# Kernel optimization log

Measured on AMD Instinct MI355X. Metric: run time of the kernel, lower is better.

The kernel has to match this reference:

```python
import jax, jax.numpy as jnp
import numpy as np


def setup_inputs() -> dict:
    key = jax.random.key(0)
    k_x, k_w, k_b = jax.random.split(key, 3)
    B, F, D, H = 4096, 64, 128, 4
    inputs = jax.random.normal(k_x, (B, F, D), dtype=jnp.float32)
    w = jax.random.normal(k_w, (H, D), dtype=jnp.float32)
    b = jax.random.normal(k_b, (H,), dtype=jnp.float32)
    return {"inputs": inputs, "w": w, "b": b}


def reference(inputs, w, b):
    # pairwise outer-product contracted with head weights:
    # scores[b,i,j,h] = sum_d x[b,i,d] * x[b,j,d] * w[h,d]
    scores = jnp.einsum('bid,bjd,hd->bijh', inputs, inputs, w) + b  # [B,F,F,H]
    s = jnp.sum(scores, axis=-1)  # [B,F,F]
    denom = jnp.sum(s, axis=(1, 2), keepdims=True)  # [B,1,1]
    return s / denom
```

## Files before the change

kernel.cpp:

```cpp
#include <hip/hip_runtime.h>
#include <hip/hip_bf16.h>


constexpr int F = 64;
constexpr int D = 128;

using bf16x8 = __attribute__((ext_vector_type(8))) short;
using f32x4  = __attribute__((ext_vector_type(4))) float;

__device__ __forceinline__ int tile_addr(int chunk, int row) {
    return ((((chunk << 6) + row) << 4) ^ ((chunk & 7) << 4));
}

__device__ __forceinline__ unsigned pk2(float lo, float hi) {
    float2 f2; f2.x = lo; f2.y = hi;
    __hip_bfloat162 h = __float22bfloat162_rn(f2);
    union { __hip_bfloat162 h2; unsigned u; } cv; cv.h2 = h;
    return cv.u;
}
__device__ __forceinline__ float lo16f(unsigned u) { return __uint_as_float(u << 16); }
__device__ __forceinline__ float hi16f(unsigned u) { return __uint_as_float(u & 0xFFFF0000u); }

__global__ __launch_bounds__(256, 8) void afm_kernel(
    const float* __restrict__ x, const float* __restrict__ w,
    const float* __restrict__ bias, float* __restrict__ out)
{
    __shared__ short sB[F * D];
    __shared__ float sW[D];
    __shared__ float sSp[4][D];

    const int t    = threadIdx.x;
    const int blk  = blockIdx.x;
    const int lane = t & 63;
    const int wv   = t >> 6;

    if (t < D) sW[t] = w[t] + w[D + t] + w[2 * D + t] + w[3 * D + t];
    const float bsum = bias[0] + bias[1] + bias[2] + bias[3];

    const float* xb = x + (size_t)blk * (F * D);
    const int col   = (4 * t) & 127;
    const int chunk = col >> 3;
    const int ebyte = (col & 7) << 1;
    float c0 = 0.f, c1 = 0.f, c2 = 0.f, c3 = 0.f;
    char* sBc = reinterpret_cast<char*>(sB);

    #pragma unroll
    for (int k = 0; k < 8; ++k) {
        const int f   = k * 1024 + 4 * t;
        const int row = f >> 7;
        const float4 v = *reinterpret_cast<const float4*>(xb + f);
        c0 += v.x; c1 += v.y; c2 += v.z; c3 += v.w;
        uint2 pb; pb.x = pk2(v.x, v.y); pb.y = pk2(v.z, v.w);
        *reinterpret_cast<uint2*>(sBc + tile_addr(chunk, row) + ebyte) = pb;
    }
    c0 += __shfl_xor(c0, 32, 64); c1 += __shfl_xor(c1, 32, 64);
    c2 += __shfl_xor(c2, 32, 64); c3 += __shfl_xor(c3, 32, 64);
    if (lane < 32) {
        float4 cs; cs.x = c0; cs.y = c1; cs.z = c2; cs.w = c3;
        *reinterpret_cast<float4*>(&sSp[wv][col]) = cs;
    }
    __syncthreads();

    const float S0 = sSp[0][lane] + sSp[1][lane] + sSp[2][lane] + sSp[3][lane];
    const float S1 = sSp[0][64 + lane] + sSp[1][64 + lane] + sSp[2][64 + lane] + sSp[3][64 + lane];
    float p = S0 * S0 * sW[lane] + S1 * S1 * sW[64 + lane];
    #pragma unroll
    for (int off = 32; off; off >>= 1) p += __shfl_xor(p, off, 64);

    f32x4 acc[4] = {{0,0,0,0},{0,0,0,0},{0,0,0,0},{0,0,0,0}};
    const int fr   = lane & 15;
    const int kgrp = lane >> 4;
    const int r_a  = wv * 16 + fr;

    #pragma unroll
    for (int s = 0; s < 4; ++s) {
        const int ch = 4 * s + kgrp;
        const uint4  raw = *reinterpret_cast<const uint4*>(sBc + tile_addr(ch, r_a));
        const float4 wa  = *reinterpret_cast<const float4*>(&sW[ch * 8]);
        const float4 wb  = *reinterpret_cast<const float4*>(&sW[ch * 8 + 4]);
        union { uint4 u; bf16x8 v; } af;
        af.u.x = pk2(lo16f(raw.x) * wa.x, hi16f(raw.x) * wa.y);
        af.u.y = pk2(lo16f(raw.y) * wa.z, hi16f(raw.y) * wa.w);
        af.u.z = pk2(lo16f(raw.z) * wb.x, hi16f(raw.z) * wb.y);
        af.u.w = pk2(lo16f(raw.w) * wb.z, hi16f(raw.w) * wb.w);
        #pragma unroll
        for (int tj = 0; tj < 4; ++tj) {
            union { uint4 u; bf16x8 v; } bf;
            bf.u = *reinterpret_cast<const uint4*>(sBc + tile_addr(ch, tj * 16 + fr));
            acc[tj] = __builtin_amdgcn_mfma_f32_16x16x32_bf16(af.v, bf.v, acc[tj], 0, 0, 0);
        }
    }

    const float rden  = 1.0f / (p + 4096.0f * bsum);
    const int   rbase = wv * 16 + 4 * kgrp;
    float* ob = out + (size_t)blk * (F * F);
    #pragma unroll
    for (int tj = 0; tj < 4; ++tj) {
        float4 o;
        o.x = (acc[tj][0] + bsum) * rden;
        o.y = (acc[tj][1] + bsum) * rden;
        o.z = (acc[tj][2] + bsum) * rden;
        o.w = (acc[tj][3] + bsum) * rden;
        *reinterpret_cast<float4*>(ob + (size_t)(tj * 16 + fr) * F + rbase) = o;
    }
}

extern "C" void kernel_launch(void* const* d_in, const int* in_sizes, int n_in,
                              void* d_out, int out_size, void* d_ws, size_t ws_size,
                              hipStream_t stream) {
    const float* x  = (const float*)d_in[0];
    const float* w  = (const float*)d_in[1];
    const float* b  = (const float*)d_in[2];
    float* out      = (float*)d_out;

    afm_kernel<<<4096, 256, 0, stream>>>(x, w, b, out);
}
```

Before: 36.02 us.

## Stage fp32 inputs into LDS via direct global-to-LDS loads with swizzle

Replaces the register path (global load, bf16 pack, LDS store) with asynchronous global_load_lds of raw fp32 rows into a swizzled LDS tile. Column sums and the bf16 conversion now read from LDS, and the B operand is converted to bf16 inside the MFMA loop. LDS use doubles to 32KB per block, so the occupancy hint is lowered to 4 blocks. The intent is to cut VGPR staging and instruction overhead on the load path, at the cost of extra LDS reads, repeated conversions of B fragments, and lower occupancy.

```diff
diff --git a/kernel.cpp b/kernel.cpp
--- a/kernel.cpp
+++ b/kernel.cpp
@@ -8,91 +8,98 @@
 using bf16x8 = __attribute__((ext_vector_type(8))) short;
 using f32x4  = __attribute__((ext_vector_type(4))) float;
 
-__device__ __forceinline__ int tile_addr(int chunk, int row) {
-    return ((((chunk << 6) + row) << 4) ^ ((chunk & 7) << 4));
-}
-
 __device__ __forceinline__ unsigned pk2(float lo, float hi) {
     float2 f2; f2.x = lo; f2.y = hi;
     __hip_bfloat162 h = __float22bfloat162_rn(f2);
     union { __hip_bfloat162 h2; unsigned u; } cv; cv.h2 = h;
     return cv.u;
 }
-__device__ __forceinline__ float lo16f(unsigned u) { return __uint_as_float(u << 16); }
-__device__ __forceinline__ float hi16f(unsigned u) { return __uint_as_float(u & 0xFFFF0000u); }
 
-__global__ __launch_bounds__(256, 8) void afm_kernel(
+__global__ __launch_bounds__(256, 4) void afm_kernel(
     const float* __restrict__ x, const float* __restrict__ w,
     const float* __restrict__ bias, float* __restrict__ out)
 {
-    __shared__ short sB[F * D];
+    __shared__ float sX[F * D];
     __shared__ float sW[D];
-    __shared__ float sSp[4][D];
+    __shared__ float sSp[8][D];
 
-    const int t    = threadIdx.x;
-    const int blk  = blockIdx.x;
-    const int lane = t & 63;
-    const int wv   = t >> 6;
+    const int t      = threadIdx.x;
+    const int blk    = blockIdx.x;
+    const int lane   = t & 63;
+    const int wv     = t >> 6;
+    const int l31    = lane & 31;
+    const int rowpar = t >> 5;
 
     if (t < D) sW[t] = w[t] + w[D + t] + w[2 * D + t] + w[3 * D + t];
     const float bsum = bias[0] + bias[1] + bias[2] + bias[3];
 
     const float* xb = x + (size_t)blk * (F * D);
-    const int col   = (4 * t) & 127;
-    const int chunk = col >> 3;
-    const int ebyte = (col & 7) << 1;
-    float c0 = 0.f, c1 = 0.f, c2 = 0.f, c3 = 0.f;
-    char* sBc = reinterpret_cast<char*>(sB);
-
+    const int cb = l31 ^ rowpar;
+    const float* srcbase = xb + rowpar * D + cb * 4;
     #pragma unroll
     for (int k = 0; k < 8; ++k) {
-        const int f   = k * 1024 + 4 * t;
-        const int row = f >> 7;
-        const float4 v = *reinterpret_cast<const float4*>(xb + f);
-        c0 += v.x; c1 += v.y; c2 += v.z; c3 += v.w;
-        uint2 pb; pb.x = pk2(v.x, v.y); pb.y = pk2(v.z, v.w);
-        *reinterpret_cast<uint2*>(sBc + tile_addr(chunk, row) + ebyte) = pb;
-    }
-    c0 += __shfl_xor(c0, 32, 64); c1 += __shfl_xor(c1, 32, 64);
-    c2 += __shfl_xor(c2, 32, 64); c3 += __shfl_xor(c3, 32, 64);
-    if (lane < 32) {
-        float4 cs; cs.x = c0; cs.y = c1; cs.z = c2; cs.w = c3;
-        *reinterpret_cast<float4*>(&sSp[wv][col]) = cs;
+        const float* src = srcbase + k * 8 * D;
+        float* dst = sX + (k * 4 + wv) * 256;
+        __builtin_amdgcn_global_load_lds(
+            (const __attribute__((address_space(1))) void*)src,
+            (__attribute__((address_space(3))) void*)dst,
+            16, 0, 0);
     }
     __syncthreads();
 
-    const float S0 = sSp[0][lane] + sSp[1][lane] + sSp[2][lane] + sSp[3][lane];
-    const float S1 = sSp[0][64 + lane] + sSp[1][64 + lane] + sSp[2][64 + lane] + sSp[3][64 + lane];
-    float p = S0 * S0 * sW[lane] + S1 * S1 * sW[64 + lane];
+    float4 c4 = {0.f, 0.f, 0.f, 0.f};
     #pragma unroll
-    for (int off = 32; off; off >>= 1) p += __shfl_xor(p, off, 64);
+    for (int k = 0; k < 8; ++k) {
+        const float4 v = *reinterpret_cast<const float4*>(sX + (k * 4 + wv) * 256 + lane * 4);
+        c4.x += v.x; c4.y += v.y; c4.z += v.z; c4.w += v.w;
+    }
+    *reinterpret_cast<float4*>(&sSp[rowpar][4 * cb]) = c4;
+    __syncthreads();
+
+    float S0 = 0.f, S1 = 0.f;
+    #pragma unroll
+    for (int p8 = 0; p8 < 8; ++p8) { S0 += sSp[p8][lane]; S1 += sSp[p8][64 + lane]; }
+    float dp = S0 * S0 * sW[lane] + S1 * S1 * sW[64 + lane];
+    #pragma unroll
+    for (int off = 32; off; off >>= 1) dp += __shfl_xor(dp, off, 64);
+    const float rden = 1.0f / (dp + 4096.0f * bsum);
 
     f32x4 acc[4] = {{0,0,0,0},{0,0,0,0},{0,0,0,0},{0,0,0,0}};
     const int fr   = lane & 15;
     const int kgrp = lane >> 4;
     const int r_a  = wv * 16 + fr;
+    const char* sXc = reinterpret_cast<const char*>(sX);
+    const int rowA = r_a * 512;
+    const int swA  = (r_a & 7) << 4;
+    const int swB  = (fr & 7) << 4;
 
     #pragma unroll
     for (int s = 0; s < 4; ++s) {
-        const int ch = 4 * s + kgrp;
-        const uint4  raw = *reinterpret_cast<const uint4*>(sBc + tile_addr(ch, r_a));
-        const float4 wa  = *reinterpret_cast<const float4*>(&sW[ch * 8]);
-        const float4 wb  = *reinterpret_cast<const float4*>(&sW[ch * 8 + 4]);
+        const int ch    = 4 * s + kgrp;
+        const int cbyte = ch * 32;
+        const int aA = rowA + (cbyte ^ swA);
+        const float4 a0 = *reinterpret_cast<const float4*>(sXc + aA);
+        const float4 a1 = *reinterpret_cast<const float4*>(sXc + (aA ^ 16));
+        const float4 wa = *reinterpret_cast<const float4*>(&sW[ch * 8]);
+        const float4 wb = *reinterpret_cast<const float4*>(&sW[ch * 8 + 4]);
         union { uint4 u; bf16x8 v; } af;
-        af.u.x = pk2(lo16f(raw.x) * wa.x, hi16f(raw.x) * wa.y);
-        af.u.y = pk2(lo16f(raw.y) * wa.z, hi16f(raw.y) * wa.w);
-        af.u.z = pk2(lo16f(raw.z) * wb.x, hi16f(raw.z) * wb.y);
-        af.u.w = pk2(lo16f(raw.w) * wb.z, hi16f(raw.w) * wb.w);
+        af.u.x = pk2(a0.x * wa.x, a0.y * wa.y);
+        af.u.y = pk2(a0.z * wa.z, a0.w * wa.w);
+        af.u.z = pk2(a1.x * wb.x, a1.y * wb.y);
+        af.u.w = pk2(a1.z * wb.z, a1.w * wb.w);
         #pragma unroll
         for (int tj = 0; tj < 4; ++tj) {
+            const int aB = (tj * 16 + fr) * 512 + (cbyte ^ swB);
+            const float4 b0 = *reinterpret_cast<const float4*>(sXc + aB);
+            const float4 b1 = *reinterpret_cast<const float4*>(sXc + (aB ^ 16));
             union { uint4 u; bf16x8 v; } bf;
-            bf.u = *reinterpret_cast<const uint4*>(sBc + tile_addr(ch, tj * 16 + fr));
+            bf.u.x = pk2(b0.x, b0.y); bf.u.y = pk2(b0.z, b0.w);
+            bf.u.z = pk2(b1.x, b1.y); bf.u.w = pk2(b1.z, b1.w);
             acc[tj] = __builtin_amdgcn_mfma_f32_16x16x32_bf16(af.v, bf.v, acc[tj], 0, 0, 0);
         }
     }
 
-    const float rden  = 1.0f / (p + 4096.0f * bsum);
-    const int   rbase = wv * 16 + 4 * kgrp;
+    const int rbase = wv * 16 + 4 * kgrp;
     float* ob = out + (size_t)blk * (F * F);
     #pragma unroll
     for (int tj = 0; tj < 4; ++tj) {
```

After: 37.00 us. 1.03x slower.

## Process four batches per block with register prefetch and double-buffered LDS

Applied to the files above, without the earlier changes.

Each block now handles four batch items in sequence instead of one and launches a quarter as many blocks. While one item is computed, the next item's global loads are issued into registers, and LDS tiles alternate between two buffers so that only one barrier is needed per item. This spreads the per-block setup (weight and bias sums) across four items and hides load latency behind compute. In exchange it raises register and LDS use, which lowers the occupancy hint from 8 to 4, and leaves 1024 blocks to cover the GPU.

```diff
diff --git a/kernel.cpp b/kernel.cpp
--- a/kernel.cpp
+++ b/kernel.cpp
@@ -21,87 +21,109 @@
 __device__ __forceinline__ float lo16f(unsigned u) { return __uint_as_float(u << 16); }
 __device__ __forceinline__ float hi16f(unsigned u) { return __uint_as_float(u & 0xFFFF0000u); }
 
-__global__ __launch_bounds__(256, 8) void afm_kernel(
+__global__ __launch_bounds__(256, 4) void afm_kernel(
     const float* __restrict__ x, const float* __restrict__ w,
     const float* __restrict__ bias, float* __restrict__ out)
 {
-    __shared__ short sB[F * D];
+    __shared__ short sB[2][F * D];
     __shared__ float sW[D];
-    __shared__ float sSp[4][D];
+    __shared__ float sSp[2][4][D];
 
     const int t    = threadIdx.x;
-    const int blk  = blockIdx.x;
     const int lane = t & 63;
     const int wv   = t >> 6;
 
     if (t < D) sW[t] = w[t] + w[D + t] + w[2 * D + t] + w[3 * D + t];
     const float bsum = bias[0] + bias[1] + bias[2] + bias[3];
 
-    const float* xb = x + (size_t)blk * (F * D);
     const int col   = (4 * t) & 127;
     const int chunk = col >> 3;
     const int ebyte = (col & 7) << 1;
-    float c0 = 0.f, c1 = 0.f, c2 = 0.f, c3 = 0.f;
-    char* sBc = reinterpret_cast<char*>(sB);
+    const int fr    = lane & 15;
+    const int kgrp  = lane >> 4;
+    const int r_a   = wv * 16 + fr;
+    const int rbase = wv * 16 + 4 * kgrp;
+
+    const size_t b0 = (size_t)blockIdx.x * 4;
+    const float* xb = x + b0 * (F * D);
+
+    float4 v[8];
+    #pragma unroll
+    for (int k = 0; k < 8; ++k)
+        v[k] = *reinterpret_cast<const float4*>(xb + k * 1024 + 4 * t);
 
     #pragma unroll
-    for (int k = 0; k < 8; ++k) {
-        const int f   = k * 1024 + 4 * t;
-        const int row = f >> 7;
-        const float4 v = *reinterpret_cast<const float4*>(xb + f);
-        c0 += v.x; c1 += v.y; c2 += v.z; c3 += v.w;
-        uint2 pb; pb.x = pk2(v.x, v.y); pb.y = pk2(v.z, v.w);
-        *reinterpret_cast<uint2*>(sBc + tile_addr(chunk, row) + ebyte) = pb;
-    }
-    c0 += __shfl_xor(c0, 32, 64); c1 += __shfl_xor(c1, 32, 64);
-    c2 += __shfl_xor(c2, 32, 64); c3 += __shfl_xor(c3, 32, 64);
-    if (lane < 32) {
-        float4 cs; cs.x = c0; cs.y = c1; cs.z = c2; cs.w = c3;
-        *reinterpret_cast<float4*>(&sSp[wv][col]) = cs;
-    }
-    __syncthreads();
+    for (int m = 0; m < 4; ++m) {
+        char* sBc = reinterpret_cast<char*>(&sB[m & 1][0]);
 
-    const float S0 = sSp[0][lane] + sSp[1][lane] + sSp[2][lane] + sSp[3][lane];
-    const float S1 = sSp[0][64 + lane] + sSp[1][64 + lane] + sSp[2][64 + lane] + sSp[3][64 + lane];
-    float p = S0 * S0 * sW[lane] + S1 * S1 * sW[64 + lane];
-    #pragma unroll
-    for (int off = 32; off; off >>= 1) p += __shfl_xor(p, off, 64);
+        float4 vn[8];
+        if (m < 3) {
+            const float* xn = xb + (size_t)(m + 1) * (F * D);
+            #pragma unroll
+            for (int k = 0; k < 8; ++k)
+                vn[k] = *reinterpret_cast<const float4*>(xn + k * 1024 + 4 * t);
+        }
 
-    f32x4 acc[4] = {{0,0,0,0},{0,0,0,0},{0,0,0,0},{0,0,0,0}};
-    const int fr   = lane & 15;
-    const int kgrp = lane >> 4;
-    const int r_a  = wv * 16 + fr;
+        float c0 = 0.f, c1 = 0.f, c2 = 0.f, c3 = 0.f;
+        #pragma unroll
+        for (int k = 0; k < 8; ++k) {
+            const int row = 8 * k + (t >> 5);
+            c0 += v[k].x; c1 += v[k].y; c2 += v[k].z; c3 += v[k].w;
+            uint2 pb; pb.x = pk2(v[k].x, v[k].y); pb.y = pk2(v[k].z, v[k].w);
+            *reinterpret_cast<uint2*>(sBc + tile_addr(chunk, row) + ebyte) = pb;
+        }
+        c0 += __shfl_xor(c0, 32, 64); c1 += __shfl_xor(c1, 32, 64);
+        c2 += __shfl_xor(c2, 32, 64); c3 += __shfl_xor(c3, 32, 64);
+        if (lane < 32) {
+            float4 cs; cs.x = c0; cs.y = c1; cs.z = c2; cs.w = c3;
+            *reinterpret_cast<float4*>(&sSp[m & 1][wv][col]) = cs;
+        }
+        __syncthreads();
 
-    #pragma unroll
-    for (int s = 0; s < 4; ++s) {
-        const int ch = 4 * s + kgrp;
-        const uint4  raw = *reinterpret_cast<const uint4*>(sBc + tile_addr(ch, r_a));
-        const float4 wa  = *reinterpret_cast<const float4*>(&sW[ch * 8]);
-        const float4 wb  = *reinterpret_cast<const float4*>(&sW[ch * 8 + 4]);
-        union { uint4 u; bf16x8 v; } af;
-        af.u.x = pk2(lo16f(raw.x) * wa.x, hi16f(raw.x) * wa.y);
-        af.u.y = pk2(lo16f(raw.y) * wa.z, hi16f(raw.y) * wa.w);
-        af.u.z = pk2(lo16f(raw.z) * wb.x, hi16f(raw.z) * wb.y);
-        af.u.w = pk2(lo16f(raw.w) * wb.z, hi16f(raw.w) * wb.w);
+        const float S0 = sSp[m & 1][0][lane] + sSp[m & 1][1][lane]
+                       + sSp[m & 1][2][lane] + sSp[m & 1][3][lane];
+        const float S1 = sSp[m & 1][0][64 + lane] + sSp[m & 1][1][64 + lane]
+                       + sSp[m & 1][2][64 + lane] + sSp[m & 1][3][64 + lane];
+        float p = S0 * S0 * sW[lane] + S1 * S1 * sW[64 + lane];
+        #pragma unroll
+        for (int off = 32; off; off >>= 1) p += __shfl_xor(p, off, 64);
+        const float rden = 1.0f / (p + 4096.0f * bsum);
+
+        f32x4 acc[4] = {{0,0,0,0},{0,0,0,0},{0,0,0,0},{0,0,0,0}};
+        #pragma unroll
+        for (int s = 0; s < 4; ++s) {
+            const int ch = 4 * s + kgrp;
+            const uint4  raw = *reinterpret_cast<const uint4*>(sBc + tile_addr(ch, r_a));
+            const float4 wa  = *reinterpret_cast<const float4*>(&sW[ch * 8]);
+            const float4 wb  = *reinterpret_cast<const float4*>(&sW[ch * 8 + 4]);
+            union { uint4 u; bf16x8 vv; } af;
+            af.u.x = pk2(lo16f(raw.x) * wa.x, hi16f(raw.x) * wa.y);
+            af.u.y = pk2(lo16f(raw.y) * wa.z, hi16f(raw.y) * wa.w);
+            af.u.z = pk2(lo16f(raw.z) * wb.x, hi16f(raw.z) * wb.y);
+            af.u.w = pk2(lo16f(raw.w) * wb.z, hi16f(raw.w) * wb.w);
+            #pragma unroll
+            for (int tj = 0; tj < 4; ++tj) {
+                union { uint4 u; bf16x8 vv; } bf;
+                bf.u = *reinterpret_cast<const uint4*>(sBc + tile_addr(ch, tj * 16 + fr));
+                acc[tj] = __builtin_amdgcn_mfma_f32_16x16x32_bf16(af.vv, bf.vv, acc[tj], 0, 0, 0);
+            }
+        }
+
+        float* ob = out + (b0 + m) * (size_t)(F * F);
         #pragma unroll
         for (int tj = 0; tj < 4; ++tj) {
-            union { uint4 u; bf16x8 v; } bf;
-            bf.u = *reinterpret_cast<const uint4*>(sBc + tile_addr(ch, tj * 16 + fr));
-            acc[tj] = __builtin_amdgcn_mfma_f32_16x16x32_bf16(af.v, bf.v, acc[tj], 0, 0, 0);
+            float4 o;
+            o.x = (acc[tj][0] + bsum) * rden;
+            o.y = (acc[tj][1] + bsum) * rden;
+            o.z = (acc[tj][2] + bsum) * rden;
+            o.w = (acc[tj][3] + bsum) * rden;
+            *reinterpret_cast<float4*>(ob + (size_t)(tj * 16 + fr) * F + rbase) = o;
         }
-    }
 
-    const float rden  = 1.0f / (p + 4096.0f * bsum);
-    const int   rbase = wv * 16 + 4 * kgrp;
-    float* ob = out + (size_t)blk * (F * F);
-    #pragma unroll
-    for (int tj = 0; tj < 4; ++tj) {
-        float4 o;
-        o.x = (acc[tj][0] + bsum) * rden;
-        o.y = (acc[tj][1] + bsum) * rden;
-        o.z = (acc[tj][2] + bsum) * rden;
-        o.w = (acc[tj][3] + bsum) * rden;
-        *reinterpret_cast<float4*>(ob + (size_t)(tj * 16 + fr) * F + rbase) = o;
+        if (m < 3) {
+            #pragma unroll
+            for (int k = 0; k < 8; ++k) v[k] = vn[k];
+        }
     }
 }
 
@@ -113,5 +135,5 @@
     const float* b  = (const float*)d_in[2];
     float* out      = (float*)d_out;
 
-    afm_kernel<<<4096, 256, 0, stream>>>(x, w, b, out);
+    afm_kernel<<<1024, 256, 0, stream>>>(x, w, b, out);
 }
```

Measured after the change: 36.55 us. About the same (+1.5%).
